# Kernel optimization log

Hardware: AMD Instinct MI355X
Metric: run time of the kernel (lower is better)

The kernel has to match this reference:

```python
import jax, jax.numpy as jnp
import numpy as np

N, X_DIM, Y_DIM, HID = 1536, 192, 192, 64


def setup_inputs() -> dict:
    key = jax.random.key(0)
    ks = jax.random.split(key, 6)
    x = jax.random.normal(ks[0], (N, X_DIM), dtype=jnp.float32)
    y = jax.random.normal(ks[1], (N, Y_DIM), dtype=jnp.float32)
    mask = jnp.ones((N, 1), dtype=bool)
    # nn.Linear default init: U(-1/sqrt(fan_in), 1/sqrt(fan_in))
    b1_bound = 1.0 / np.sqrt(X_DIM + Y_DIM)
    b2_bound = 1.0 / np.sqrt(HID)
    W1 = jax.random.uniform(ks[2], (HID, X_DIM + Y_DIM), jnp.float32, -b1_bound, b1_bound)
    b1 = jax.random.uniform(ks[3], (HID,), jnp.float32, -b1_bound, b1_bound)
    W2 = jax.random.uniform(ks[4], (1, HID), jnp.float32, -b2_bound, b2_bound)
    b2 = jax.random.uniform(ks[5], (1,), jnp.float32, -b2_bound, b2_bound)
    return {"x_samples": x, "y_samples": y, "W1": W1, "b1": b1, "W2": W2, "b2": b2, "mask": mask}


def reference(x_samples, y_samples, W1, b1, W2, b2, mask):
    # mask is all-True by construction -> masking is identity (static shapes).
    n = x_samples.shape[0]
    d_x = x_samples.shape[1]
    W1x, W1y = W1[:, :d_x], W1[:, d_x:]
    hx = x_samples @ W1x.T          # [N, H]
    hy = y_samples @ W1y.T          # [N, H]
    # T0: paired (i,i) samples
    h0 = jax.nn.relu(hx + hy + b1)                       # [N, H]
    T0 = jax.nn.softplus(h0 @ W2.T + b2)                 # [N, 1]
    # T1: all pairs; row i = y_i, col j = x_j (matches x_tile/y_tile repeat pattern)
    h1 = jax.nn.relu(hy[:, None, :] + hx[None, :, :] + b1)   # [N, N, H]
    T1 = jax.nn.softplus(jnp.einsum('ijh,oh->ij', h1, W2) + b2[0])  # [N, N]
    lse = jax.nn.logsumexp(T1, axis=1)                   # [N]
    lower_bound = T0.mean() - (lse.mean() - jnp.log(jnp.float32(n)))
    return -lower_bound
```

## Files before the change

### kernel.cpp

```cpp
#include <hip/hip_runtime.h>
#include <hip/hip_bf16.h>
#include <math.h>

#define N_    1536
#define HID_  64
#define DX_   192
#define JW_   16
#define JCH_  (N_ / JW_)
#define IB_   (N_ / 64)

__global__ __launch_bounds__(256) void k1(
    const float* __restrict__ x, const float* __restrict__ y,
    const float* __restrict__ W1, const float* __restrict__ b1,
    const float* __restrict__ W2, const float* __restrict__ b2,
    float* __restrict__ Am, float* __restrict__ Bm,
    float* __restrict__ cv, float* __restrict__ dv, float* __restrict__ wp)
{
    __shared__ float4 w1t[48 * 64];
    int t = threadIdx.x;
    int h = t & 63;
    int w = t >> 6;
    bool aSide = (blockIdx.x < 96);

    const float4* w1row = (const float4*)(W1 + h * (2 * DX_) + (aSide ? DX_ : 0));
    int kq0 = w * 12;
    #pragma unroll
    for (int q = 0; q < 12; ++q)
        w1t[(kq0 + q) * 64 + h] = w1row[kq0 + q];
    __syncthreads();

    int row0 = (blockIdx.x % 96) * 16;
    const float* inp = aSide ? y : x;
    float b1h = aSide ? b1[h] : 0.f;
    float wph = 0.5f * W2[h];
    float b2v = b2[0];

    #pragma unroll
    for (int p = 0; p < 4; ++p) {
        int row = row0 + p * 4 + w;
        const float4* in4 = (const float4*)(inp + row * DX_);
        float acc = b1h;
        #pragma unroll
        for (int q = 0; q < 48; ++q) {
            float4 wv = w1t[q * 64 + h];
            float4 iv = in4[q];
            acc = fmaf(iv.x, wv.x, acc);
            acc = fmaf(iv.y, wv.y, acc);
            acc = fmaf(iv.z, wv.z, acc);
            acc = fmaf(iv.w, wv.w, acc);
        }
        (aSide ? Am : Bm)[row * HID_ + h] = acc;

        float v = wph * acc;
        #pragma unroll
        for (int m = 32; m; m >>= 1) v += __shfl_xor(v, m, 64);
        if (h == 0) {
            if (aSide) cv[row] = v + b2v;
            else       dv[row] = v;
        }
    }
    if (blockIdx.x == 0 && t < 64) wp[t] = 0.5f * W2[t];
}

__global__ __launch_bounds__(256) void k2(
    const float* __restrict__ Am, const float* __restrict__ Bm,
    const float* __restrict__ wp, const float* __restrict__ cv,
    const float* __restrict__ dv,
    float* __restrict__ part, float* __restrict__ t0)
{
    int lane = threadIdx.x & 63;
    int sub  = threadIdx.x >> 6;
    int jc   = blockIdx.x % JCH_;
    int ib   = (blockIdx.x / JCH_) * 4 + sub;
    int i    = ib * 64 + lane;

    float a[HID_];
    #pragma unroll
    for (int q = 0; q < HID_ / 4; ++q)
        ((float4*)a)[q] = ((const float4*)(Am + i * HID_))[q];

    float wv[HID_];
    #pragma unroll
    for (int q = 0; q < HID_ / 4; ++q)
        ((float4*)wv)[q] = ((const float4*)wp)[q];

    float ci = cv[i];
    float se = 0.f;

    for (int jj = 0; jj < JW_; ++jj) {
        int j = jc * JW_ + jj;
        float p0 = ci + dv[j];
        float p1 = 0.f;
        const float4* Br = (const float4*)(Bm + j * HID_);
        #pragma unroll
        for (int q = 0; q < HID_ / 4; ++q) {
            float4 t = Br[q];
            p0 = fmaf(wv[4*q+0], fabsf(a[4*q+0] + t.x), p0);
            p1 = fmaf(wv[4*q+1], fabsf(a[4*q+1] + t.y), p1);
            p0 = fmaf(wv[4*q+2], fabsf(a[4*q+2] + t.z), p0);
            p1 = fmaf(wv[4*q+3], fabsf(a[4*q+3] + t.w), p1);
        }
        float p = p0 + p1;
        se += __expf(p);
        if (j == i) {
            t0[i] = fmaxf(p, 0.f) + log1pf(__expf(-fabsf(p)));
        }
    }
    part[jc * N_ + i] = se;
}

__global__ __launch_bounds__(64) void k3a(
    const float* __restrict__ part, const float* __restrict__ t0,
    double* __restrict__ red)
{
    int i = blockIdx.x * 64 + threadIdx.x;
    double s = (double)N_;
    for (int jc = 0; jc < JCH_; ++jc) s += (double)part[jc * N_ + i];
    double v = log(s) - (double)t0[i];
    #pragma unroll
    for (int m = 32; m; m >>= 1) v += __shfl_xor(v, m, 64);
    if (threadIdx.x == 0) red[blockIdx.x] = v;
}

__global__ __launch_bounds__(64) void k3b(
    const double* __restrict__ red, float* __restrict__ out)
{
    double v = (threadIdx.x < IB_) ? red[threadIdx.x] : 0.0;
    #pragma unroll
    for (int m = 32; m; m >>= 1) v += __shfl_xor(v, m, 64);
    if (threadIdx.x == 0)
        out[0] = (float)(v / (double)N_ - log((double)N_));
}

extern "C" void kernel_launch(void* const* d_in, const int* in_sizes, int n_in,
                              void* d_out, int out_size, void* d_ws, size_t ws_size,
                              hipStream_t stream)
{
    const float* x  = (const float*)d_in[0];
    const float* y  = (const float*)d_in[1];
    const float* W1 = (const float*)d_in[2];
    const float* b1 = (const float*)d_in[3];
    const float* W2 = (const float*)d_in[4];
    const float* b2 = (const float*)d_in[5];

    double* red = (double*)d_ws;
    float* ws   = (float*)d_ws + 64;
    float* Am   = ws;
    float* Bm   = Am + N_ * HID_;
    float* cv   = Bm + N_ * HID_;
    float* dv   = cv + N_;
    float* wp   = dv + N_;
    float* part = wp + HID_;
    float* t0   = part + JCH_ * N_;

    hipLaunchKernelGGL(k1, dim3(192), dim3(256), 0, stream,
                       x, y, W1, b1, W2, b2, Am, Bm, cv, dv, wp);
    hipLaunchKernelGGL(k2, dim3((IB_ / 4) * JCH_), dim3(256), 0, stream,
                       Am, Bm, wp, cv, dv, part, t0);
    hipLaunchKernelGGL(k3a, dim3(IB_), dim3(64), 0, stream, part, t0, red);
    hipLaunchKernelGGL(k3b, dim3(1), dim3(64), 0, stream, red, (float*)d_out);
}
```

Measured before the change: 42.29 us.

## Use packed relu-max pair math in all-pairs kernel and transpose A matrix

The all-pairs inner loop switches from the |a+b| identity (with precomputed linear terms cv/dv) to a direct relu via packed two-wide max and fma, so the compiler can emit packed FP32 instructions. The A-side hidden matrix is stored transposed so per-thread loads coalesce across lanes, W2 is read directly, and the k1 reductions for cv/dv/wp are removed. The j-chunk width drops from 16 to 12, which gives more blocks and a larger partial-sum buffer for k3a to reduce. Packed-math codegen is not guaranteed, and the extra max per element could cost more than the removed precomputation.

```diff
diff --git a/kernel.cpp b/kernel.cpp
--- a/kernel.cpp
+++ b/kernel.cpp
@@ -5,16 +5,16 @@
 #define N_    1536
 #define HID_  64
 #define DX_   192
-#define JW_   16
+#define JW_   12
 #define JCH_  (N_ / JW_)
 #define IB_   (N_ / 64)
+
+typedef float v2f __attribute__((ext_vector_type(2)));
 
 __global__ __launch_bounds__(256) void k1(
     const float* __restrict__ x, const float* __restrict__ y,
     const float* __restrict__ W1, const float* __restrict__ b1,
-    const float* __restrict__ W2, const float* __restrict__ b2,
-    float* __restrict__ Am, float* __restrict__ Bm,
-    float* __restrict__ cv, float* __restrict__ dv, float* __restrict__ wp)
+    float* __restrict__ AmT, float* __restrict__ Bm)
 {
     __shared__ float4 w1t[48 * 64];
     int t = threadIdx.x;
@@ -32,8 +32,6 @@
     int row0 = (blockIdx.x % 96) * 16;
     const float* inp = aSide ? y : x;
     float b1h = aSide ? b1[h] : 0.f;
-    float wph = 0.5f * W2[h];
-    float b2v = b2[0];
 
     #pragma unroll
     for (int p = 0; p < 4; ++p) {
@@ -49,23 +47,14 @@
             acc = fmaf(iv.z, wv.z, acc);
             acc = fmaf(iv.w, wv.w, acc);
         }
-        (aSide ? Am : Bm)[row * HID_ + h] = acc;
-
-        float v = wph * acc;
-        #pragma unroll
-        for (int m = 32; m; m >>= 1) v += __shfl_xor(v, m, 64);
-        if (h == 0) {
-            if (aSide) cv[row] = v + b2v;
-            else       dv[row] = v;
-        }
+        if (aSide) AmT[h * N_ + row] = acc;
+        else       Bm[row * HID_ + h] = acc;
     }
-    if (blockIdx.x == 0 && t < 64) wp[t] = 0.5f * W2[t];
 }
 
 __global__ __launch_bounds__(256) void k2(
-    const float* __restrict__ Am, const float* __restrict__ Bm,
-    const float* __restrict__ wp, const float* __restrict__ cv,
-    const float* __restrict__ dv,
+    const float* __restrict__ AmT, const float* __restrict__ Bm,
+    const float* __restrict__ W2, const float* __restrict__ b2,
     float* __restrict__ part, float* __restrict__ t0)
 {
     int lane = threadIdx.x & 63;
@@ -74,33 +63,31 @@
     int ib   = (blockIdx.x / JCH_) * 4 + sub;
     int i    = ib * 64 + lane;
 
-    float a[HID_];
+    v2f a2[HID_ / 2];
     #pragma unroll
-    for (int q = 0; q < HID_ / 4; ++q)
-        ((float4*)a)[q] = ((const float4*)(Am + i * HID_))[q];
+    for (int h2 = 0; h2 < HID_ / 2; ++h2) {
+        a2[h2].x = AmT[(2 * h2 + 0) * N_ + i];
+        a2[h2].y = AmT[(2 * h2 + 1) * N_ + i];
+    }
 
-    float wv[HID_];
-    #pragma unroll
-    for (int q = 0; q < HID_ / 4; ++q)
-        ((float4*)wv)[q] = ((const float4*)wp)[q];
-
-    float ci = cv[i];
+    const v2f* Wr = (const v2f*)W2;
+    float b2v = b2[0];
     float se = 0.f;
 
     for (int jj = 0; jj < JW_; ++jj) {
         int j = jc * JW_ + jj;
-        float p0 = ci + dv[j];
-        float p1 = 0.f;
-        const float4* Br = (const float4*)(Bm + j * HID_);
+        const v2f* Br = (const v2f*)(Bm + j * HID_);
+        v2f acc0 = {0.f, 0.f}, acc1 = {0.f, 0.f};
         #pragma unroll
-        for (int q = 0; q < HID_ / 4; ++q) {
-            float4 t = Br[q];
-            p0 = fmaf(wv[4*q+0], fabsf(a[4*q+0] + t.x), p0);
-            p1 = fmaf(wv[4*q+1], fabsf(a[4*q+1] + t.y), p1);
-            p0 = fmaf(wv[4*q+2], fabsf(a[4*q+2] + t.z), p0);
-            p1 = fmaf(wv[4*q+3], fabsf(a[4*q+3] + t.w), p1);
+        for (int q = 0; q < HID_ / 2; q += 2) {
+            v2f s0 = a2[q]     + Br[q];
+            v2f s1 = a2[q + 1] + Br[q + 1];
+            v2f r0 = __builtin_elementwise_max(s0, (v2f){0.f, 0.f});
+            v2f r1 = __builtin_elementwise_max(s1, (v2f){0.f, 0.f});
+            acc0 = __builtin_elementwise_fma(Wr[q],     r0, acc0);
+            acc1 = __builtin_elementwise_fma(Wr[q + 1], r1, acc1);
         }
-        float p = p0 + p1;
+        float p = (acc0.x + acc0.y) + (acc1.x + acc1.y) + b2v;
         se += __expf(p);
         if (j == i) {
             t0[i] = fmaxf(p, 0.f) + log1pf(__expf(-fabsf(p)));
@@ -143,20 +130,17 @@
     const float* W2 = (const float*)d_in[4];
     const float* b2 = (const float*)d_in[5];
 
-    double* red = (double*)d_ws;
-    float* ws   = (float*)d_ws + 64;
-    float* Am   = ws;
-    float* Bm   = Am + N_ * HID_;
-    float* cv   = Bm + N_ * HID_;
-    float* dv   = cv + N_;
-    float* wp   = dv + N_;
-    float* part = wp + HID_;
-    float* t0   = part + JCH_ * N_;
+    double* red  = (double*)d_ws;
+    float*  ws   = (float*)d_ws + 64;
+    float*  AmT  = ws;
+    float*  Bm   = AmT + HID_ * N_;
+    float*  part = Bm + N_ * HID_;
+    float*  t0   = part + JCH_ * N_;
 
     hipLaunchKernelGGL(k1, dim3(192), dim3(256), 0, stream,
-                       x, y, W1, b1, W2, b2, Am, Bm, cv, dv, wp);
+                       x, y, W1, b1, AmT, Bm);
     hipLaunchKernelGGL(k2, dim3((IB_ / 4) * JCH_), dim3(256), 0, stream,
-                       Am, Bm, wp, cv, dv, part, t0);
+                       AmT, Bm, W2, b2, part, t0);
     hipLaunchKernelGGL(k3a, dim3(IB_), dim3(64), 0, stream, part, t0, red);
     hipLaunchKernelGGL(k3b, dim3(1), dim3(64), 0, stream, red, (float*)d_out);
 }
```

Result: slower. 49.15 us (+16.2%).
